# Kernel optimization log

Measured on AMD Instinct MI355X. Metric: run time of the kernel, lower is better.

## Reference

```python
import jax, jax.numpy as jnp
import numpy as np

N_NODES = 50000
N_EDGES = 1600000
IN_DIM, HIDDEN, OUT_DIM = 128, 128, 64


def setup_inputs() -> dict:
    key = jax.random.key(0)
    ks = jax.random.split(key, 8)
    x = jax.random.normal(ks[0], (N_NODES, IN_DIM), dtype=jnp.float32)
    edge_index = jax.random.randint(ks[1], (2, N_EDGES), 0, N_NODES, dtype=jnp.int64)
    # SAGEConv params: lin_l applied to aggregated neighbors (with bias),
    # lin_r applied to root/self features (no bias) -- PyG defaults.
    def lin_init(k, fan_in, fan_out):
        bound = 1.0 / np.sqrt(fan_in)
        return jax.random.uniform(k, (fan_in, fan_out), jnp.float32, -bound, bound)
    W1_l = lin_init(ks[2], IN_DIM, HIDDEN)
    W1_r = lin_init(ks[3], IN_DIM, HIDDEN)
    b1 = jnp.zeros((HIDDEN,), jnp.float32)
    W2_l = lin_init(ks[4], HIDDEN, OUT_DIM)
    W2_r = lin_init(ks[5], HIDDEN, OUT_DIM)
    b2 = jnp.zeros((OUT_DIM,), jnp.float32)
    return {"x": x, "edge_index": edge_index, "W1_l": W1_l, "W1_r": W1_r,
            "b1": b1, "W2_l": W2_l, "W2_r": W2_r, "b2": b2}


def _sage_conv(h, src, dst, n_nodes, W_l, W_r, b):
    # gather messages from source nodes, mean-aggregate at destinations
    msg = h[src]                                              # [E, D]
    agg_sum = jax.ops.segment_sum(msg, dst, num_segments=n_nodes)
    deg = jax.ops.segment_sum(jnp.ones((src.shape[0],), h.dtype), dst,
                              num_segments=n_nodes)
    agg_mean = agg_sum / jnp.maximum(deg, 1.0)[:, None]       # [N, D]
    return agg_mean @ W_l + h @ W_r + b


def reference(x, edge_index, W1_l, W1_r, b1, W2_l, W2_r, b2):
    n = x.shape[0]
    src, dst = edge_index[0], edge_index[1]
    h = jax.nn.relu(_sage_conv(x, src, dst, n, W1_l, W1_r, b1))
    return _sage_conv(h, src, dst, n, W2_l, W2_r, b2)
```

## Files before the change

### kernel.cpp

```cpp
#include <hip/hip_runtime.h>

#define NN 50000
#define NE 1600000
#define BSTRIDE 96
#define C_BKT 196
#define P1_BLKS 512
#define P1_CHUNK 3125
#define CAP 56
#define XCVT_BLKS 1563
#define WCVT_BLKS 48
#define PP_PREP (XCVT_BLKS + WCVT_BLKS)
#define RGRP 3128

typedef __bf16 bf16x8 __attribute__((ext_vector_type(8)));
typedef float  f32x4  __attribute__((ext_vector_type(4)));
typedef float  f32x2  __attribute__((ext_vector_type(2)));

__device__ __forceinline__ float bfLo(uint u) { union { uint i; float f; } v; v.i = u << 16; return v.f; }
__device__ __forceinline__ float bfHi(uint u) { union { uint i; float f; } v; v.i = u & 0xffff0000u; return v.f; }
__device__ __forceinline__ ushort f2bf(float f) {
    union { float f; uint i; } v; v.f = f;
    uint r = v.i + 0x7fffu + ((v.i >> 16) & 1u);
    return (ushort)(r >> 16);
}
__device__ __forceinline__ uint pack2(float a, float b) {
    return (uint)f2bf(a) | ((uint)f2bf(b) << 16);
}
__device__ __forceinline__ bf16x8 load8(const ushort* p) {
    union { uint4 u; bf16x8 b; } v; v.u = *(const uint4*)p; return v.b;
}

#define ACC8(u) { a0 += bfLo(u.x); a1 += bfHi(u.x); a2 += bfLo(u.y); a3 += bfHi(u.y); \
                  a4 += bfLo(u.z); a5 += bfHi(u.z); a6 += bfLo(u.w); a7 += bfHi(u.w); }

#define CVA(u, o) { f32x2 p0 = __builtin_amdgcn_cvt_pk_f32_fp8((int)(u), 0); \
                    f32x2 p1 = __builtin_amdgcn_cvt_pk_f32_fp8((int)(u), 1); \
                    a[(o)+0] += p0.x; a[(o)+1] += p0.y; a[(o)+2] += p1.x; a[(o)+3] += p1.y; }
#define ACCF8(v) { CVA((v).x, 0); CVA((v).y, 4); CVA((v).z, 8); CVA((v).w, 12); }

__device__ __forceinline__ int pkOff(int n, int k) {
    return (((n >> 4) * 4 + (k >> 5)) * 512) + (((k >> 3) & 3) * 128) + ((n & 15) * 8) + (k & 7);
}

__global__ __launch_bounds__(1024) void k_pp(
    const float4* __restrict__ x, ushort* __restrict__ xbp, uint* __restrict__ xf8,
    const float* __restrict__ W1l, const float* __restrict__ W1r,
    const float* __restrict__ W2l, const float* __restrict__ W2r,
    ushort* __restrict__ T1l, ushort* __restrict__ T1r,
    ushort* __restrict__ T2l, ushort* __restrict__ T2r,
    const int* __restrict__ src, const int* __restrict__ dst,
    uint* __restrict__ cells, ushort* __restrict__ cnt) {
    __shared__ uint hist[C_BKT];
    const int b = blockIdx.x;
    const int tid = threadIdx.x;
    if (b < XCVT_BLKS) {
        int i = b * 1024 + tid;
        if (i < NN * 128 / 4) {
            float4 v = x[i];
            int r = i >> 5, k0 = (i & 31) * 4;
            ushort4 o; o.x = f2bf(v.x); o.y = f2bf(v.y); o.z = f2bf(v.z); o.w = f2bf(v.w);
            *(ushort4*)(xbp + pkOff(r, k0)) = o;
            uint rr = (uint)__builtin_amdgcn_cvt_pk_fp8_f32(v.x, v.y, 0, 0);
            rr = (uint)__builtin_amdgcn_cvt_pk_fp8_f32(v.z, v.w, (int)rr, 1);
            xf8[i] = rr;
        }
    } else if (b < PP_PREP) {
        int i = (b - XCVT_BLKS) * 1024 + tid;
        if (i < 16384) {
            int k = i >> 7, n = i & 127; T1l[pkOff(n, k)] = f2bf(W1l[i]);
        } else if (i < 32768) {
            int j = i - 16384; int k = j >> 7, n = j & 127; T1r[pkOff(n, k)] = f2bf(W1r[j]);
        } else if (i < 40960) {
            int j = i - 32768; int k = j >> 6, n = j & 63;  T2l[pkOff(n, k)] = f2bf(W2l[j]);
        } else {
            int j = i - 40960; int k = j >> 6, n = j & 63;  T2r[pkOff(n, k)] = f2bf(W2r[j]);
        }
    } else {
        const int b2 = b - PP_PREP;
        for (int i = tid; i < C_BKT; i += 1024) hist[i] = 0;
        __syncthreads();
        const int beg = b2 * P1_CHUNK;
        uint* myCells = cells + (size_t)b2 * C_BKT * CAP;
        for (int i = beg + tid; i < beg + P1_CHUNK; i += 1024) {
            int d = dst[i];
            int s = src[i];
            int c = d >> 8;
            uint p = atomicAdd(&hist[c], 1);
            if (p < CAP) myCells[c * CAP + p] = ((uint)(d & 255) << 16) | (uint)s;
        }
        __syncthreads();
        for (int i = tid; i < C_BKT; i += 1024)
            cnt[(size_t)b2 * C_BKT + i] = (ushort)min(hist[i], (uint)CAP);
    }
}

__global__ __launch_bounds__(1024) void k_part2(const uint* __restrict__ cells,
                        const ushort* __restrict__ cnt,
                        ushort* __restrict__ col, int* __restrict__ deg) {
    __shared__ uint hist[256];
    const int c = blockIdx.x;
    if (threadIdx.x < 256) hist[threadIdx.x] = 0;
    __syncthreads();
    const int b = threadIdx.x >> 1;
    const int sub = threadIdx.x & 1;
    const uint* cell = cells + ((size_t)b * C_BKT + c) * CAP;
    const int n = cnt[(size_t)b * C_BKT + c];
    const int nodeBase = c << 8;
    for (int j = sub; j < n; j += 2) {
        uint e = cell[j];
        int dl = e >> 16;
        uint p = atomicAdd(&hist[dl], 1);
        if (p < BSTRIDE)
            col[(size_t)(nodeBase + dl) * BSTRIDE + p] = (ushort)(e & 0xFFFF);
    }
    __syncthreads();
    if (threadIdx.x < 256) {
        int node = nodeBase + threadIdx.x;
        if (node < NN) deg[node] = (int)hist[threadIdx.x];
    }
}

__global__ void k_agg128(const uchar* __restrict__ xf8, const ushort* __restrict__ col,
                         const int* __restrict__ deg, ushort* __restrict__ aggp) {
    int node = (blockIdx.x * blockDim.x + threadIdx.x) >> 6;
    int lane = threadIdx.x & 63;
    int q = lane >> 3;
    int c = lane & 7;
    int d = deg[node];
    int dd = min(d, BSTRIDE);
    const ushort* cb = col + (size_t)node * BSTRIDE;
    float a[16];
    #pragma unroll
    for (int i = 0; i < 16; i++) a[i] = 0.f;
    for (int j0 = 0; j0 < dd; j0 += 64) {
        int idx = (j0 + lane < dd) ? (int)cb[j0 + lane] : 0;
        int cnt = min(64, dd - j0);
        int t = 0;
        for (; t + 16 <= cnt; t += 16) {
            int s0 = __shfl(idx, t + q);
            int s1 = __shfl(idx, t + 8 + q);
            uint4 u0 = *(const uint4*)(xf8 + (size_t)s0 * 128 + c * 16);
            uint4 u1 = *(const uint4*)(xf8 + (size_t)s1 * 128 + c * 16);
            ACCF8(u0); ACCF8(u1);
        }
        for (; t < cnt; t += 8) {
            int s = __shfl(idx, t + q);
            if (t + q < cnt) {
                uint4 u = *(const uint4*)(xf8 + (size_t)s * 128 + c * 16);
                ACCF8(u);
            }
        }
    }
    #pragma unroll
    for (int m = 8; m < 64; m <<= 1) {
        #pragma unroll
        for (int i = 0; i < 16; i++) a[i] += __shfl_xor(a[i], m);
    }
    if (q == 0) {
        float inv = 1.f / fmaxf((float)d, 1.f);
        int base = ((node >> 4) * 4 + (c >> 1)) * 512 + ((c & 1) * 2) * 128 + (node & 15) * 8;
        uint4 o;
        o.x = pack2(a[0] * inv, a[1] * inv);
        o.y = pack2(a[2] * inv, a[3] * inv);
        o.z = pack2(a[4] * inv, a[5] * inv);
        o.w = pack2(a[6] * inv, a[7] * inv);
        *(uint4*)(aggp + base) = o;
        o.x = pack2(a[8] * inv, a[9] * inv);
        o.y = pack2(a[10] * inv, a[11] * inv);
        o.z = pack2(a[12] * inv, a[13] * inv);
        o.w = pack2(a[14] * inv, a[15] * inv);
        *(uint4*)(aggp + base + 128) = o;
    }
}

#define PAD1 136
__global__ __launch_bounds__(256) void k_gemm12(
    const ushort* __restrict__ aggp, const ushort* __restrict__ xbp,
    const ushort* __restrict__ T1l, const ushort* __restrict__ T1r,
    const ushort* __restrict__ T2l, const ushort* __restrict__ T2r,
    const float* __restrict__ b1, const float* __restrict__ b2,
    ushort* __restrict__ hW, float* __restrict__ outp) {
    __shared__ ushort hS[2][16 * PAD1];
    const int lane = threadIdx.x & 63;
    const int wave = threadIdx.x >> 6;
    const int s = wave >> 1;
    const int ch = wave & 1;
    const int quad = lane >> 4, r16 = lane & 15;
    const int row0 = blockIdx.x * 32 + s * 16;
    const int g = blockIdx.x * 2 + s;
    ushort* myS = &hS[s][0];

    f32x4 acc[4];
    #pragma unroll
    for (int nt = 0; nt < 4; nt++) acc[nt] = (f32x4){0.f, 0.f, 0.f, 0.f};
    #pragma unroll
    for (int kt = 0; kt < 4; kt++) {
        bf16x8 aAgg = load8(aggp + (size_t)(g * 4 + kt) * 512 + lane * 8);
        bf16x8 aXb  = load8(xbp  + (size_t)(g * 4 + kt) * 512 + lane * 8);
        #pragma unroll
        for (int nt = 0; nt < 4; nt++) {
            const int tile = ((ch * 4 + nt) * 4 + kt) * 512 + lane * 8;
            acc[nt] = __builtin_amdgcn_mfma_f32_16x16x32_bf16(aAgg, load8(T1l + tile), acc[nt], 0, 0, 0);
            acc[nt] = __builtin_amdgcn_mfma_f32_16x16x32_bf16(aXb,  load8(T1r + tile), acc[nt], 0, 0, 0);
        }
    }
    #pragma unroll
    for (int nt = 0; nt < 4; nt++) {
        int cc = ch * 64 + nt * 16 + r16;
        float bv = b1[cc];
        #pragma unroll
        for (int i = 0; i < 4; i++)
            myS[(quad * 4 + i) * PAD1 + cc] = f2bf(fmaxf(acc[nt][i] + bv, 0.f));
    }
    __syncthreads();

    f32x4 acc2[2], acc3[2];
    #pragma unroll
    for (int nt = 0; nt < 2; nt++) {
        acc2[nt] = (f32x4){0.f, 0.f, 0.f, 0.f};
        acc3[nt] = (f32x4){0.f, 0.f, 0.f, 0.f};
    }
    #pragma unroll
    for (int kt = 0; kt < 4; kt++) {
        bf16x8 ah = load8(&myS[r16 * PAD1 + kt * 32 + quad * 8]);
        #pragma unroll
        for (int nt = 0; nt < 2; nt++) {
            const int tile = ((ch * 2 + nt) * 4 + kt) * 512 + lane * 8;
            acc2[nt] = __builtin_amdgcn_mfma_f32_16x16x32_bf16(ah, load8(T2l + tile), acc2[nt], 0, 0, 0);
            acc3[nt] = __builtin_amdgcn_mfma_f32_16x16x32_bf16(ah, load8(T2r + tile), acc3[nt], 0, 0, 0);
        }
    }
    #pragma unroll
    for (int nt = 0; nt < 2; nt++) {
        int cc = ch * 32 + nt * 16 + r16;
        float bv = b2[cc];
        #pragma unroll
        for (int i = 0; i < 4; i++) {
            int rr = row0 + quad * 4 + i;
            if (rr < NN) {
                hW[(size_t)rr * 64 + cc] = f2bf(acc2[nt][i]);
                outp[(size_t)rr * 64 + cc] = acc3[nt][i] + bv;
            }
        }
    }
}

__global__ void k_agg64f(const ushort* __restrict__ hW, const ushort* __restrict__ col,
                         const int* __restrict__ deg, const float* __restrict__ outp,
                         float* __restrict__ out) {
    int node = (blockIdx.x * blockDim.x + threadIdx.x) >> 6;
    int lane = threadIdx.x & 63;
    int q = lane >> 3;
    int c = lane & 7;
    int d = deg[node];
    int dd = min(d, BSTRIDE);
    const ushort* cb = col + (size_t)node * BSTRIDE;
    float a0=0.f,a1=0.f,a2=0.f,a3=0.f,a4=0.f,a5=0.f,a6=0.f,a7=0.f;
    for (int j0 = 0; j0 < dd; j0 += 64) {
        int idx = (j0 + lane < dd) ? (int)cb[j0 + lane] : 0;
        int cnt = min(64, dd - j0);
        int t = 0;
        for (; t + 16 <= cnt; t += 16) {
            int s0 = __shfl(idx, t + q);
            int s1 = __shfl(idx, t + 8 + q);
            uint4 u0 = *(const uint4*)(hW + (size_t)s0 * 64 + c * 8);
            uint4 u1 = *(const uint4*)(hW + (size_t)s1 * 64 + c * 8);
            ACC8(u0); ACC8(u1);
        }
        for (; t < cnt; t += 8) {
            int s = __shfl(idx, t + q);
            if (t + q < cnt) {
                uint4 u = *(const uint4*)(hW + (size_t)s * 64 + c * 8);
                ACC8(u);
            }
        }
    }
    #pragma unroll
    for (int m = 8; m < 64; m <<= 1) {
        a0 += __shfl_xor(a0, m); a1 += __shfl_xor(a1, m);
        a2 += __shfl_xor(a2, m); a3 += __shfl_xor(a3, m);
        a4 += __shfl_xor(a4, m); a5 += __shfl_xor(a5, m);
        a6 += __shfl_xor(a6, m); a7 += __shfl_xor(a7, m);
    }
    if (q == 0) {
        float inv = 1.f / fmaxf((float)d, 1.f);
        float4 p0 = *(const float4*)(outp + (size_t)node * 64 + c * 8);
        float4 p1 = *(const float4*)(outp + (size_t)node * 64 + c * 8 + 4);
        float4 o;
        o.x = a0 * inv + p0.x; o.y = a1 * inv + p0.y;
        o.z = a2 * inv + p0.z; o.w = a3 * inv + p0.w;
        *(float4*)(out + (size_t)node * 64 + c * 8) = o;
        o.x = a4 * inv + p1.x; o.y = a5 * inv + p1.y;
        o.z = a6 * inv + p1.z; o.w = a7 * inv + p1.w;
        *(float4*)(out + (size_t)node * 64 + c * 8 + 4) = o;
    }
}

extern "C" void kernel_launch(void* const* d_in, const int* in_sizes, int n_in,
                              void* d_out, int out_size, void* d_ws, size_t ws_size,
                              hipStream_t stream) {
    const float* x   = (const float*)d_in[0];
    const int*   ei  = (const int*)d_in[1];
    const float* W1l = (const float*)d_in[2];
    const float* W1r = (const float*)d_in[3];
    const float* b1  = (const float*)d_in[4];
    const float* W2l = (const float*)d_in[5];
    const float* W2r = (const float*)d_in[6];
    const float* b2  = (const float*)d_in[7];
    float* out = (float*)d_out;

    const int* src = ei;
    const int* dst = ei + NE;

    char* w = (char*)d_ws;
    ushort* col   = (ushort*)w;                  w += (size_t)NN * BSTRIDE * 2;
    int* deg      = (int*)w;                     w += (size_t)50048 * 4;
    ushort* cnt   = (ushort*)w;                  w += (size_t)P1_BLKS * C_BKT * 2;
    ushort* xbp   = (ushort*)w;                  w += (size_t)RGRP * 2048 * 2;
    ushort* T1l   = (ushort*)w;                  w += 128 * 128 * 2;
    ushort* T1r   = (ushort*)w;                  w += 128 * 128 * 2;
    ushort* T2l   = (ushort*)w;                  w += 64 * 128 * 2;
    ushort* T2r   = (ushort*)w;                  w += 64 * 128 * 2;
    ushort* aggp  = (ushort*)w;                  w += (size_t)RGRP * 2048 * 2;
    ushort* hW    = (ushort*)w;                  w += (size_t)NN * 64 * 2;
    float* outp   = (float*)w;                   w += (size_t)NN * 64 * 4;
    uchar* xf8    = (uchar*)w;                   w += (size_t)NN * 128;
    uint* cells  = (uint*)aggp;

    k_pp<<<PP_PREP + P1_BLKS, 1024, 0, stream>>>(
        (const float4*)x, xbp, (uint*)xf8, W1l, W1r, W2l, W2r,
        T1l, T1r, T2l, T2r, src, dst, cells, cnt);
    k_part2<<<C_BKT, 1024, 0, stream>>>(cells, cnt, col, deg);

    k_agg128<<<NN / 4, 256, 0, stream>>>(xf8, col, deg, aggp);
    k_gemm12<<<(NN + 31) / 32, 256, 0, stream>>>(aggp, xbp, T1l, T1r, T2l, T2r, b1, b2, hW, outp);

    k_agg64f<<<NN / 4, 256, 0, stream>>>(hW, col, deg, outp, out);
}
```

Measured before the change: 198.5 us.

## Fuse CSR bucket build with first-layer aggregation using shared-memory column lists

Merges the second partitioning pass and the layer-1 neighbor aggregation into one kernel: each block scatters edges for 200 destination nodes into a shared-memory column table, writes col/deg out for layer 2, then aggregates fp8 features directly from the shared lists. Bucket width changes from 256 to 200 nodes and per-cell capacity shrinks, and cells get a dedicated buffer since aggp is now written concurrently. This removes a launch and a global read of col/deg, but runs the aggregation with only 250 large blocks, reducing parallelism for a latency-bound gather.

```diff
diff --git a/kernel.cpp b/kernel.cpp
--- a/kernel.cpp
+++ b/kernel.cpp
@@ -3,10 +3,11 @@
 #define NN 50000
 #define NE 1600000
 #define BSTRIDE 96
-#define C_BKT 196
+#define BNODES 200
+#define C_BKT 250
 #define P1_BLKS 512
 #define P1_CHUNK 3125
-#define CAP 56
+#define CAP 48
 #define XCVT_BLKS 1563
 #define WCVT_BLKS 48
 #define PP_PREP (XCVT_BLKS + WCVT_BLKS)
@@ -84,9 +85,9 @@
         for (int i = beg + tid; i < beg + P1_CHUNK; i += 1024) {
             int d = dst[i];
             int s = src[i];
-            int c = d >> 8;
+            int c = d / BNODES;
             uint p = atomicAdd(&hist[c], 1);
-            if (p < CAP) myCells[c * CAP + p] = ((uint)(d & 255) << 16) | (uint)s;
+            if (p < CAP) myCells[c * CAP + p] = ((uint)(d - c * BNODES) << 16) | (uint)s;
         }
         __syncthreads();
         for (int i = tid; i < C_BKT; i += 1024)
@@ -94,82 +95,85 @@
     }
 }
 
-__global__ __launch_bounds__(1024) void k_part2(const uint* __restrict__ cells,
-                        const ushort* __restrict__ cnt,
-                        ushort* __restrict__ col, int* __restrict__ deg) {
-    __shared__ uint hist[256];
+__global__ __launch_bounds__(1024) void k_pagg(
+    const uint* __restrict__ cells, const ushort* __restrict__ cnt,
+    const uchar* __restrict__ xf8, ushort* __restrict__ col,
+    int* __restrict__ deg, ushort* __restrict__ aggp) {
+    __shared__ uint hist[BNODES];
+    __shared__ ushort colS[BNODES * BSTRIDE];
     const int c = blockIdx.x;
-    if (threadIdx.x < 256) hist[threadIdx.x] = 0;
+    const int tid = threadIdx.x;
+    if (tid < BNODES) hist[tid] = 0;
     __syncthreads();
-    const int b = threadIdx.x >> 1;
-    const int sub = threadIdx.x & 1;
-    const uint* cell = cells + ((size_t)b * C_BKT + c) * CAP;
-    const int n = cnt[(size_t)b * C_BKT + c];
-    const int nodeBase = c << 8;
-    for (int j = sub; j < n; j += 2) {
-        uint e = cell[j];
-        int dl = e >> 16;
-        uint p = atomicAdd(&hist[dl], 1);
-        if (p < BSTRIDE)
-            col[(size_t)(nodeBase + dl) * BSTRIDE + p] = (ushort)(e & 0xFFFF);
+    {
+        const int b = tid >> 1, sub = tid & 1;
+        const uint* cell = cells + ((size_t)b * C_BKT + c) * CAP;
+        const int n = cnt[(size_t)b * C_BKT + c];
+        for (int j = sub; j < n; j += 2) {
+            uint e = cell[j];
+            int dl = e >> 16;
+            uint p = atomicAdd(&hist[dl], 1);
+            if (p < BSTRIDE) colS[dl * BSTRIDE + p] = (ushort)(e & 0xFFFF);
+        }
     }
     __syncthreads();
-    if (threadIdx.x < 256) {
-        int node = nodeBase + threadIdx.x;
-        if (node < NN) deg[node] = (int)hist[threadIdx.x];
-    }
-}
-
-__global__ void k_agg128(const uchar* __restrict__ xf8, const ushort* __restrict__ col,
-                         const int* __restrict__ deg, ushort* __restrict__ aggp) {
-    int node = (blockIdx.x * blockDim.x + threadIdx.x) >> 6;
-    int lane = threadIdx.x & 63;
-    int q = lane >> 3;
-    int c = lane & 7;
-    int d = deg[node];
-    int dd = min(d, BSTRIDE);
-    const ushort* cb = col + (size_t)node * BSTRIDE;
-    float a[16];
-    #pragma unroll
-    for (int i = 0; i < 16; i++) a[i] = 0.f;
-    for (int j0 = 0; j0 < dd; j0 += 64) {
-        int idx = (j0 + lane < dd) ? (int)cb[j0 + lane] : 0;
-        int cnt = min(64, dd - j0);
-        int t = 0;
-        for (; t + 16 <= cnt; t += 16) {
-            int s0 = __shfl(idx, t + q);
-            int s1 = __shfl(idx, t + 8 + q);
-            uint4 u0 = *(const uint4*)(xf8 + (size_t)s0 * 128 + c * 16);
-            uint4 u1 = *(const uint4*)(xf8 + (size_t)s1 * 128 + c * 16);
-            ACCF8(u0); ACCF8(u1);
-        }
-        for (; t < cnt; t += 8) {
-            int s = __shfl(idx, t + q);
-            if (t + q < cnt) {
-                uint4 u = *(const uint4*)(xf8 + (size_t)s * 128 + c * 16);
-                ACCF8(u);
+    const int nodeBase = c * BNODES;
+    if (tid < BNODES) deg[nodeBase + tid] = (int)hist[tid];
+    {
+        uint4* cg = (uint4*)(col + (size_t)nodeBase * BSTRIDE);
+        const uint4* cs = (const uint4*)colS;
+        for (int i = tid; i < BNODES * BSTRIDE / 8; i += 1024) cg[i] = cs[i];
+    }
+    const int wave = tid >> 6, lane = tid & 63;
+    const int q = lane >> 3;
+    const int cc = lane & 7;
+    for (int ln = wave; ln < BNODES; ln += 16) {
+        int d = (int)hist[ln];
+        int dd = min(d, BSTRIDE);
+        const ushort* cb = &colS[ln * BSTRIDE];
+        float a[16];
+        #pragma unroll
+        for (int i = 0; i < 16; i++) a[i] = 0.f;
+        for (int j0 = 0; j0 < dd; j0 += 64) {
+            int idx = (j0 + lane < dd) ? (int)cb[j0 + lane] : 0;
+            int cnt2 = min(64, dd - j0);
+            int t = 0;
+            for (; t + 16 <= cnt2; t += 16) {
+                int s0 = __shfl(idx, t + q);
+                int s1 = __shfl(idx, t + 8 + q);
+                uint4 u0 = *(const uint4*)(xf8 + (size_t)s0 * 128 + cc * 16);
+                uint4 u1 = *(const uint4*)(xf8 + (size_t)s1 * 128 + cc * 16);
+                ACCF8(u0); ACCF8(u1);
             }
-        }
-    }
-    #pragma unroll
-    for (int m = 8; m < 64; m <<= 1) {
-        #pragma unroll
-        for (int i = 0; i < 16; i++) a[i] += __shfl_xor(a[i], m);
-    }
-    if (q == 0) {
-        float inv = 1.f / fmaxf((float)d, 1.f);
-        int base = ((node >> 4) * 4 + (c >> 1)) * 512 + ((c & 1) * 2) * 128 + (node & 15) * 8;
-        uint4 o;
-        o.x = pack2(a[0] * inv, a[1] * inv);
-        o.y = pack2(a[2] * inv, a[3] * inv);
-        o.z = pack2(a[4] * inv, a[5] * inv);
-        o.w = pack2(a[6] * inv, a[7] * inv);
-        *(uint4*)(aggp + base) = o;
-        o.x = pack2(a[8] * inv, a[9] * inv);
-        o.y = pack2(a[10] * inv, a[11] * inv);
-        o.z = pack2(a[12] * inv, a[13] * inv);
-        o.w = pack2(a[14] * inv, a[15] * inv);
-        *(uint4*)(aggp + base + 128) = o;
+            for (; t < cnt2; t += 8) {
+                int s = __shfl(idx, t + q);
+                if (t + q < cnt2) {
+                    uint4 u = *(const uint4*)(xf8 + (size_t)s * 128 + cc * 16);
+                    ACCF8(u);
+                }
+            }
+        }
+        #pragma unroll
+        for (int m = 8; m < 64; m <<= 1) {
+            #pragma unroll
+            for (int i = 0; i < 16; i++) a[i] += __shfl_xor(a[i], m);
+        }
+        if (q == 0) {
+            int node = nodeBase + ln;
+            float inv = 1.f / fmaxf((float)d, 1.f);
+            int base = ((node >> 4) * 4 + (cc >> 1)) * 512 + ((cc & 1) * 2) * 128 + (node & 15) * 8;
+            uint4 o;
+            o.x = pack2(a[0] * inv, a[1] * inv);
+            o.y = pack2(a[2] * inv, a[3] * inv);
+            o.z = pack2(a[4] * inv, a[5] * inv);
+            o.w = pack2(a[6] * inv, a[7] * inv);
+            *(uint4*)(aggp + base) = o;
+            o.x = pack2(a[8] * inv, a[9] * inv);
+            o.y = pack2(a[10] * inv, a[11] * inv);
+            o.z = pack2(a[12] * inv, a[13] * inv);
+            o.w = pack2(a[14] * inv, a[15] * inv);
+            *(uint4*)(aggp + base + 128) = o;
+        }
     }
 }
 
@@ -325,14 +329,14 @@
     ushort* hW    = (ushort*)w;                  w += (size_t)NN * 64 * 2;
     float* outp   = (float*)w;                   w += (size_t)NN * 64 * 4;
     uchar* xf8    = (uchar*)w;                   w += (size_t)NN * 128;
-    uint* cells  = (uint*)aggp;
+    uint* cells   = (uint*)w;                    w += (size_t)P1_BLKS * C_BKT * CAP * 4;
 
     k_pp<<<PP_PREP + P1_BLKS, 1024, 0, stream>>>(
         (const float4*)x, xbp, (uint*)xf8, W1l, W1r, W2l, W2r,
         T1l, T1r, T2l, T2r, src, dst, cells, cnt);
-    k_part2<<<C_BKT, 1024, 0, stream>>>(cells, cnt, col, deg);
-
-    k_agg128<<<NN / 4, 256, 0, stream>>>(xf8, col, deg, aggp);
+
+    k_pagg<<<C_BKT, 1024, 0, stream>>>(cells, cnt, xf8, col, deg, aggp);
+
     k_gemm12<<<(NN + 31) / 32, 256, 0, stream>>>(aggp, xbp, T1l, T1r, T2l, T2r, b1, b2, hW, outp);
 
     k_agg64f<<<NN / 4, 256, 0, stream>>>(hW, col, deg, outp, out);
```

Result: no change. 198.8 us (+0.2%).
